# Optimization experiments

Measured on AMD Instinct MI355X. Metric: run time of the kernel, lower is better.

The kernel has to match this reference:

```python
import jax, jax.numpy as jnp
import numpy as np

DIM = 100      # number of assets in the basket
M = 50         # time steps
T = 1.0
R = 0.05
SIGMA = 0.2
S0 = 100.0
DT = T / M
H = 128        # hidden_dim of ZetaNetwork
B = 8192       # Monte-Carlo paths (batch)
EPS = 1e-5     # torch LayerNorm eps


def _layernorm(x, g, b):
    mu = jnp.mean(x, axis=-1, keepdims=True)
    var = jnp.mean((x - mu) ** 2, axis=-1, keepdims=True)
    return (x - mu) / jnp.sqrt(var + EPS) * g + b


def setup_inputs() -> dict:
    key = jax.random.key(0)
    ks = jax.random.split(key, 12)
    dw = jax.random.normal(ks[0], (B, M, DIM), dtype=jnp.float32)
    t_grid = jax.random.uniform(ks[1], (B, M), dtype=jnp.float32)
    s = 0.05
    inp = {
        "dw": dw,
        "t_grid": t_grid,
        "W1": jax.random.normal(ks[2], (DIM + 1, H), dtype=jnp.float32) * s,
        "b1": jnp.zeros((H,), jnp.float32),
        "g1": jnp.ones((H,), jnp.float32),
        "be1": jnp.zeros((H,), jnp.float32),
        "W2": jax.random.normal(ks[3], (H, H), dtype=jnp.float32) * s,
        "b2": jnp.zeros((H,), jnp.float32),
        "g2": jnp.ones((H,), jnp.float32),
        "be2": jnp.zeros((H,), jnp.float32),
        "W3": jax.random.normal(ks[4], (H, H), dtype=jnp.float32) * s,
        "b3": jnp.zeros((H,), jnp.float32),
        "g3": jnp.ones((H,), jnp.float32),
        "be3": jnp.zeros((H,), jnp.float32),
        "W4": jax.random.normal(ks[5], (H, DIM), dtype=jnp.float32) * s,
        "b4": jnp.zeros((DIM,), jnp.float32),
        "Y0": jnp.array([10.0], dtype=jnp.float32),
    }
    return inp


def reference(dw, t_grid, W1, b1, g1, be1, W2, b2, g2, be2,
              W3, b3, g3, be3, W4, b4, Y0):
    batch = dw.shape[0]

    def zeta_net(x):  # x: [B, DIM+1]
        h = jax.nn.gelu(_layernorm(x @ W1 + b1, g1, be1), approximate=False)
        h = jax.nn.gelu(_layernorm(h @ W2 + b2, g2, be2), approximate=False)
        h = jax.nn.gelu(_layernorm(h @ W3 + b3, g3, be3), approximate=False)
        return jax.nn.sigmoid(h @ W4 + b4)  # [B, DIM]

    def step(carry, xs):
        S, Y = carry
        dw_i, t_i = xs                                   # [B,DIM], [B,1]
        net_in = jnp.concatenate([S / S0, t_i], axis=1)  # [B,DIM+1]
        zeta = zeta_net(net_in)
        dS = S * (R * DT + SIGMA * dw_i)
        portfolio_gain = jnp.sum(zeta * dS, axis=1, keepdims=True)
        asset_val = jnp.sum(zeta * S, axis=1, keepdims=True)
        Y = Y + R * (Y - asset_val) * DT + portfolio_gain
        S = S + dS
        return (S, Y), None

    S_init = jnp.full((batch, DIM), S0, dtype=dw.dtype)
    Y_init = jnp.ones((batch, 1), dtype=dw.dtype) * Y0
    xs = (jnp.swapaxes(dw, 0, 1),                # [M,B,DIM]
          jnp.swapaxes(t_grid, 0, 1)[..., None])  # [M,B,1]
    (S, Y), _ = jax.lax.scan(step, (S_init, Y_init), xs)
    return (Y, S)
```

## Files before the change

### kernel.cpp

```cpp
#include <hip/hip_runtime.h>
#include <hip/hip_bf16.h>
#include <cstdint>
#include <cstddef>

typedef __attribute__((ext_vector_type(8))) short short8;
typedef __attribute__((ext_vector_type(4))) float f32x4;
typedef __attribute__((ext_vector_type(2))) float f32x2;
typedef __attribute__((ext_vector_type(4))) unsigned int u32x4;

#define NDIM 100
#define NSTEP 50
#define NPATH 8192
#define XSTR 128
#define ESTR 128

typedef const __attribute__((address_space(1))) unsigned int glb_u32;
typedef __attribute__((address_space(3))) unsigned int lds_u32;

__device__ __forceinline__ unsigned short f2b(float f){
  unsigned int u = __float_as_uint(f);
  u += 0x7fffu + ((u >> 16) & 1u);
  return (unsigned short)(u >> 16);
}
__device__ __forceinline__ float b2f(unsigned short h){
  return __uint_as_float(((unsigned int)h) << 16);
}

template<int CTRL>
__device__ __forceinline__ float dpp_add(float x){
  int t = __builtin_amdgcn_update_dpp(0, __float_as_int(x), CTRL, 0xF, 0xF, true);
  return x + __int_as_float(t);
}
__device__ __forceinline__ float rowsum16(float x){
  x = dpp_add<0x128>(x);
  x = dpp_add<0x124>(x);
  x = dpp_add<0x122>(x);
  x = dpp_add<0x121>(x);
  return x;
}

__global__ __launch_bounds__(256) void prep_weights(
    const float* __restrict__ W1, const float* __restrict__ W2,
    const float* __restrict__ W3, const float* __restrict__ W4,
    unsigned short* __restrict__ WTS)
{
  int idx = blockIdx.x * 256 + threadIdx.x;
  int j = idx & 7;
  int s = (idx >> 3) & 15;
  int n = (idx >> 7) & 127;
  int L = idx >> 14;
  int lc = s ^ (n & 15);
  int k  = j * 16 + lc;
  float v;
  if (L == 0)      v = (k <= NDIM) ? W1[k * 128 + n] : 0.f;
  else if (L == 1) v = W2[k * 128 + n];
  else if (L == 2) v = W3[k * 128 + n];
  else             v = (n < NDIM) ? W4[k * NDIM + n] : 0.f;
  WTS[idx] = f2b(v);
}

__global__ __launch_bounds__(256) void prep_params(
    const float* __restrict__ b1, const float* __restrict__ g1, const float* __restrict__ be1,
    const float* __restrict__ b2, const float* __restrict__ g2, const float* __restrict__ be2,
    const float* __restrict__ b3, const float* __restrict__ g3, const float* __restrict__ be3,
    const float* __restrict__ b4, float* __restrict__ PPAR)
{
  int idx = blockIdx.x * 256 + threadIdx.x;
  if (idx >= 1536) return;
  int ct = idx & 7;
  int c  = (idx >> 3) & 15;
  int p  = (idx >> 7) % 3;
  int L  = idx / 384;
  int col = ct * 16 + c;
  const float* v;
  if (L == 0)      v = (p == 0) ? b1 : (p == 1) ? g1 : be1;
  else if (L == 1) v = (p == 0) ? b2 : (p == 1) ? g2 : be2;
  else if (L == 2) v = (p == 0) ? b3 : (p == 1) ? g3 : be3;
  else             v = b4;
  float val;
  if (L == 3) val = (p == 0 && col < NDIM) ? b4[col] : 0.f;
  else        val = v[col];
  PPAR[idx] = val;
}

__global__ __launch_bounds__(256) void phaseA(
    const float* __restrict__ dw, const float* __restrict__ tg,
    unsigned short* __restrict__ X, unsigned short* __restrict__ E,
    float* __restrict__ Sout, int path0)
{
  const int pb = threadIdx.x >> 6;
  const int t  = threadIdx.x & 63;
  const int bl = blockIdx.x * 4 + pb;
  const int b  = path0 + bl;
  const int d0 = (t & 7) * 16 + (t >> 3);
  const int d1 = d0 + 8;
  float s0 = 100.f, s1 = 100.f;
  const float* dwb = dw + (long)b * NSTEP * NDIM;
  const float* tgb = tg + (long)b * NSTEP;
  unsigned short* Xb = X + (long)bl * NSTEP * XSTR;
  unsigned short* Eb = E + (long)bl * NSTEP * ESTR;
  for (int i = 0; i < NSTEP; ++i){
    float tv = tgb[i];
    float w0 = (d0 < NDIM) ? dwb[i * NDIM + d0] : 0.f;
    float w1 = (d1 < NDIM) ? dwb[i * NDIM + d1] : 0.f;
    unsigned short* Xr = Xb + i * XSTR;
    unsigned short* Er = Eb + i * ESTR;
    Xr[t]      = (d0 < NDIM) ? f2b(s0 * 0.01f) : ((d0 == NDIM) ? f2b(tv) : (unsigned short)0);
    Xr[t + 64] = (d1 < NDIM) ? f2b(s1 * 0.01f) : (unsigned short)0;
    Er[t]      = (d0 < NDIM) ? f2b(0.2f * s0 * w0) : (unsigned short)0;
    Er[t + 64] = (d1 < NDIM) ? f2b(0.2f * s1 * w1) : (unsigned short)0;
    s0 = fmaf(s0, 0.001f + 0.2f * w0, s0);
    s1 = fmaf(s1, 0.001f + 0.2f * w1, s1);
  }
  if (d0 < NDIM) Sout[(long)b * NDIM + d0] = s0;
  if (d1 < NDIM) Sout[(long)b * NDIM + d1] = s1;
}

__global__ __launch_bounds__(256, 3) void phaseB(
    const unsigned short* __restrict__ X,
    const unsigned short* __restrict__ E,
    const unsigned short* __restrict__ WTS,
    const float* __restrict__ PPAR,
    float* __restrict__ cbuf, long row0)
{
  __shared__ __align__(16) char lds[49152];
  char* const wbuf = lds;
  const int tid = threadIdx.x;
  const int w = tid >> 6;
  const int l = tid & 63;
  const int g = l >> 4;
  const int c = l & 15;
  char* const H = lds + 32768 + w * 4096;
  const long base = (long)blockIdx.x * 128 + w * 16;

  auto stage = [&](int Loff){
    #pragma unroll
    for (int it = 0; it < 8; ++it){
      int chunk = w * 8 + it;
      __builtin_amdgcn_global_load_lds((glb_u32*)(WTS + Loff + chunk * 512 + l * 8),
          (lds_u32*)(wbuf + chunk * 1024), 16, 0, 0);
    }
  };

  short8 af0[4], af1[4];
  {
    const unsigned short* xr0 = X + (base + c) * XSTR;
    const unsigned short* xr1 = X + (base + 64 + c) * XSTR;
    #pragma unroll
    for (int ks = 0; ks < 4; ++ks){
      af0[ks] = *(const short8*)(xr0 + 32 * ks + 8 * g);
      af1[ks] = *(const short8*)(xr1 + 32 * ks + 8 * g);
    }
  }

  auto mfma2 = [&](f32x4 (&acc0)[8], f32x4 (&acc1)[8], f32x4 blo, f32x4 bhi){
    #pragma unroll
    for (int ct = 0; ct < 8; ++ct){
      float bs = (ct < 4) ? blo[ct] : bhi[ct - 4];
      f32x4 z; z[0] = bs; z[1] = bs; z[2] = bs; z[3] = bs;
      acc0[ct] = z; acc1[ct] = z;
      const char* rowp = wbuf + ((ct * 16 + c) << 8);
      #pragma unroll
      for (int ks = 0; ks < 4; ++ks){
        short8 bf = *(const short8*)(rowp + (((4 * ks + g) ^ c) << 4));
        acc0[ct] = __builtin_amdgcn_mfma_f32_16x16x32_bf16(af0[ks], bf, acc0[ct], 0, 0, 0);
        acc1[ct] = __builtin_amdgcn_mfma_f32_16x16x32_bf16(af1[ks], bf, acc1[ct], 0, 0, 0);
      }
    }
  };

  auto gelu2 = [&](f32x2 y) -> f32x2 {
    f32x2 a = y * -2.4554673f;
    f32x2 u;
    u[0] = __builtin_amdgcn_exp2f(a[0]);
    u[1] = __builtin_amdgcn_exp2f(a[1]);
    f32x2 d = u + 1.0f;
    f32x2 r;
    r[0] = __builtin_amdgcn_rcpf(d[0]);
    r[1] = __builtin_amdgcn_rcpf(d[1]);
    return y * r;
  };

  auto postproc = [&](f32x4 (&acc)[8], short8 (&af)[4],
                      f32x4 glo, f32x4 ghi, f32x4 belo, f32x4 behi){
    f32x2 sA = {0.f, 0.f}, sB = {0.f, 0.f}, qA = {0.f, 0.f}, qB = {0.f, 0.f};
    #pragma unroll
    for (int ct = 0; ct < 8; ++ct){
      f32x2 xy = __builtin_shufflevector(acc[ct], acc[ct], 0, 1);
      f32x2 zw = __builtin_shufflevector(acc[ct], acc[ct], 2, 3);
      sA += xy; qA += xy * xy;
      sB += zw; qB += zw * zw;
    }
    sA[0] = rowsum16(sA[0]); sA[1] = rowsum16(sA[1]);
    sB[0] = rowsum16(sB[0]); sB[1] = rowsum16(sB[1]);
    qA[0] = rowsum16(qA[0]); qA[1] = rowsum16(qA[1]);
    qB[0] = rowsum16(qB[0]); qB[1] = rowsum16(qB[1]);
    f32x2 muA = sA * 0.0078125f, muB = sB * 0.0078125f;
    f32x2 vA = qA * 0.0078125f - muA * muA + 1e-5f;
    f32x2 vB = qB * 0.0078125f - muB * muB + 1e-5f;
    f32x2 rA, rB;
    rA[0] = rsqrtf(vA[0]); rA[1] = rsqrtf(vA[1]);
    rB[0] = rsqrtf(vB[0]); rB[1] = rsqrtf(vB[1]);
    u32x4 ov0, ov1, ov2, ov3;
    #pragma unroll
    for (int p = 0; p < 4; ++p){
      float ga0 = (p < 2) ? glo[2*p]     : ghi[2*p - 4];
      float ga1 = (p < 2) ? glo[2*p + 1] : ghi[2*p - 3];
      float be0 = (p < 2) ? belo[2*p]     : behi[2*p - 4];
      float be1 = (p < 2) ? belo[2*p + 1] : behi[2*p - 3];
      f32x2 xyE = __builtin_shufflevector(acc[2*p],   acc[2*p],   0, 1);
      f32x2 zwE = __builtin_shufflevector(acc[2*p],   acc[2*p],   2, 3);
      f32x2 xyO = __builtin_shufflevector(acc[2*p+1], acc[2*p+1], 0, 1);
      f32x2 zwO = __builtin_shufflevector(acc[2*p+1], acc[2*p+1], 2, 3);
      f32x2 AEA = rA * ga0, AEB = rB * ga0;
      f32x2 AOA = rA * ga1, AOB = rB * ga1;
      f32x2 hEA = gelu2(xyE * AEA + (be0 - muA * AEA));
      f32x2 hEB = gelu2(zwE * AEB + (be0 - muB * AEB));
      f32x2 hOA = gelu2(xyO * AOA + (be1 - muA * AOA));
      f32x2 hOB = gelu2(zwO * AOB + (be1 - muB * AOB));
      unsigned int k0, k1, k2, k3;
      asm("v_cvt_pk_bf16_f32 %0, %1, %2" : "=v"(k0) : "v"(hEA[0]), "v"(hOA[0]));
      asm("v_cvt_pk_bf16_f32 %0, %1, %2" : "=v"(k1) : "v"(hEA[1]), "v"(hOA[1]));
      asm("v_cvt_pk_bf16_f32 %0, %1, %2" : "=v"(k2) : "v"(hEB[0]), "v"(hOB[0]));
      asm("v_cvt_pk_bf16_f32 %0, %1, %2" : "=v"(k3) : "v"(hEB[1]), "v"(hOB[1]));
      ov0[p] = k0; ov1[p] = k1; ov2[p] = k2; ov3[p] = k3;
    }
    int r0 = 4 * g;
    *(u32x4*)(H + (r0 + 0) * 256 + ((c ^ (r0 + 0)) << 4)) = ov0;
    *(u32x4*)(H + (r0 + 1) * 256 + ((c ^ (r0 + 1)) << 4)) = ov1;
    *(u32x4*)(H + (r0 + 2) * 256 + ((c ^ (r0 + 2)) << 4)) = ov2;
    *(u32x4*)(H + (r0 + 3) * 256 + ((c ^ (r0 + 3)) << 4)) = ov3;
    #pragma unroll
    for (int ks = 0; ks < 4; ++ks)
      af[ks] = *(const short8*)(H + c * 256 + (((4 * ks + g) ^ c) << 4));
  };

  auto epilogue = [&](f32x4 (&acc)[8], short8 (&ep)[4], long rbase){
    f32x2 pgA = {0.f, 0.f}, pgB = {0.f, 0.f};
    #pragma unroll
    for (int ct = 0; ct < 8; ++ct){
      f32x2 xy = __builtin_shufflevector(acc[ct], acc[ct], 0, 1);
      f32x2 zw = __builtin_shufflevector(acc[ct], acc[ct], 2, 3);
      f32x2 aA = xy * -1.4426950f, aB = zw * -1.4426950f;
      f32x2 u, d, r;
      u[0] = __builtin_amdgcn_exp2f(aA[0]); u[1] = __builtin_amdgcn_exp2f(aA[1]);
      d = u + 1.f;
      r[0] = __builtin_amdgcn_rcpf(d[0]); r[1] = __builtin_amdgcn_rcpf(d[1]);
      f32x2 eA = { b2f((unsigned short)ep[0][ct]), b2f((unsigned short)ep[1][ct]) };
      pgA += r * eA;
      u[0] = __builtin_amdgcn_exp2f(aB[0]); u[1] = __builtin_amdgcn_exp2f(aB[1]);
      d = u + 1.f;
      r[0] = __builtin_amdgcn_rcpf(d[0]); r[1] = __builtin_amdgcn_rcpf(d[1]);
      f32x2 eB = { b2f((unsigned short)ep[2][ct]), b2f((unsigned short)ep[3][ct]) };
      pgB += r * eB;
    }
    pgA[0] = rowsum16(pgA[0]); pgA[1] = rowsum16(pgA[1]);
    pgB[0] = rowsum16(pgB[0]); pgB[1] = rowsum16(pgB[1]);
    if (c == 0){
      cbuf[row0 + rbase + 4 * g + 0] = pgA[0];
      cbuf[row0 + rbase + 4 * g + 1] = pgA[1];
      cbuf[row0 + rbase + 4 * g + 2] = pgB[0];
      cbuf[row0 + rbase + 4 * g + 3] = pgB[1];
    }
  };

  stage(0);
  __syncthreads();

  #pragma unroll
  for (int L = 0; L < 3; ++L){
    const float* pp = PPAR + L * 384 + c * 8;
    f32x4 blo  = *(const f32x4*)pp,         bhi  = *(const f32x4*)(pp + 4);
    f32x4 acc0[8], acc1[8];
    mfma2(acc0, acc1, blo, bhi);
    f32x4 glo  = *(const f32x4*)(pp + 128), ghi  = *(const f32x4*)(pp + 132);
    f32x4 belo = *(const f32x4*)(pp + 256), behi = *(const f32x4*)(pp + 260);
    __syncthreads();
    stage((L + 1) * 16384);
    postproc(acc0, af0, glo, ghi, belo, behi);
    postproc(acc1, af1, glo, ghi, belo, behi);
    __syncthreads();
  }

  {
    const float* pp = PPAR + 3 * 384 + c * 8;
    f32x4 blo = *(const f32x4*)pp, bhi = *(const f32x4*)(pp + 4);
    short8 ep0[4], ep1[4];
    #pragma unroll
    for (int j = 0; j < 4; ++j){
      ep0[j] = *(const short8*)(E + (base + 4 * g + j) * ESTR + c * 8);
      ep1[j] = *(const short8*)(E + (base + 64 + 4 * g + j) * ESTR + c * 8);
    }
    f32x4 acc0[8], acc1[8];
    mfma2(acc0, acc1, blo, bhi);
    epilogue(acc0, ep0, base);
    epilogue(acc1, ep1, base + 64);
  }
}

__global__ __launch_bounds__(256) void phaseC(const float* __restrict__ cbuf,
                                              const float* __restrict__ Y0,
                                              float* __restrict__ Yout)
{
  int b = blockIdx.x * 256 + threadIdx.x;
  if (b >= NPATH) return;
  const float kk = 1.0f + 0.05f * (1.0f / 50.0f);
  float y = Y0[0];
  const float* cb = cbuf + (long)b * NSTEP;
  #pragma unroll 10
  for (int i = 0; i < NSTEP; ++i) y = y * kk + cb[i];
  Yout[b] = y;
}

extern "C" void kernel_launch(void* const* d_in, const int* in_sizes, int n_in,
                              void* d_out, int out_size, void* d_ws, size_t ws_size,
                              hipStream_t stream)
{
  const float* dw  = (const float*)d_in[0];
  const float* tg  = (const float*)d_in[1];
  const float* W1  = (const float*)d_in[2];
  const float* b1  = (const float*)d_in[3];
  const float* g1  = (const float*)d_in[4];
  const float* be1 = (const float*)d_in[5];
  const float* W2  = (const float*)d_in[6];
  const float* b2  = (const float*)d_in[7];
  const float* g2  = (const float*)d_in[8];
  const float* be2 = (const float*)d_in[9];
  const float* W3  = (const float*)d_in[10];
  const float* b3  = (const float*)d_in[11];
  const float* g3  = (const float*)d_in[12];
  const float* be3 = (const float*)d_in[13];
  const float* W4  = (const float*)d_in[14];
  const float* b4  = (const float*)d_in[15];
  const float* Y0  = (const float*)d_in[16];
  float* out = (float*)d_out;

  char* ws = (char*)d_ws;
  unsigned short* WTS = (unsigned short*)ws;
  float* PPAR = (float*)(ws + 131072);
  float* cbuf = (float*)(ws + 137344);
  char* chunk = ws + 1775744;

  prep_weights<<<256, 256, 0, stream>>>(W1, W2, W3, W4, WTS);
  prep_params<<<6, 256, 0, stream>>>(b1, g1, be1, b2, g2, be2, b3, g3, be3, b4, PPAR);

  long avail = (long)ws_size - 1775744L;
  long pc = (avail > 0) ? (avail / 25600L) : 0;
  if (pc > 8192) pc = 8192;
  pc -= pc % 128;
  if (pc < 128) pc = 128;

  for (long p0 = 0; p0 < 8192; p0 += pc){
    long np = 8192 - p0; if (np > pc) np = pc;
    unsigned short* Xc = (unsigned short*)chunk;
    unsigned short* Ec = Xc + np * 50L * XSTR;
    phaseA<<<(int)(np / 4), 256, 0, stream>>>(dw, tg, Xc, Ec, out + 8192, (int)p0);
    long nrows = np * 50L;
    phaseB<<<(int)(nrows / 128), 256, 0, stream>>>(Xc, Ec, WTS, PPAR, cbuf, p0 * 50L);
  }
  phaseC<<<32, 256, 0, stream>>>(cbuf, Y0, out);
}
```

Baseline: 201.5 us.

## Fuse phaseA and phaseB into one software-pipelined kernel over double-buffered chunks

```diff
diff --git a/kernel.cpp b/kernel.cpp
--- a/kernel.cpp
+++ b/kernel.cpp
@@ -83,47 +83,53 @@
   PPAR[idx] = val;
 }
 
-__global__ __launch_bounds__(256) void phaseA(
+__global__ __launch_bounds__(256, 3) void fusedAB(
     const float* __restrict__ dw, const float* __restrict__ tg,
-    unsigned short* __restrict__ X, unsigned short* __restrict__ E,
-    float* __restrict__ Sout, int path0)
-{
-  const int pb = threadIdx.x >> 6;
-  const int t  = threadIdx.x & 63;
-  const int bl = blockIdx.x * 4 + pb;
-  const int b  = path0 + bl;
-  const int d0 = (t & 7) * 16 + (t >> 3);
-  const int d1 = d0 + 8;
-  float s0 = 100.f, s1 = 100.f;
-  const float* dwb = dw + (long)b * NSTEP * NDIM;
-  const float* tgb = tg + (long)b * NSTEP;
-  unsigned short* Xb = X + (long)bl * NSTEP * XSTR;
-  unsigned short* Eb = E + (long)bl * NSTEP * ESTR;
-  for (int i = 0; i < NSTEP; ++i){
-    float tv = tgb[i];
-    float w0 = (d0 < NDIM) ? dwb[i * NDIM + d0] : 0.f;
-    float w1 = (d1 < NDIM) ? dwb[i * NDIM + d1] : 0.f;
-    unsigned short* Xr = Xb + i * XSTR;
-    unsigned short* Er = Eb + i * ESTR;
-    Xr[t]      = (d0 < NDIM) ? f2b(s0 * 0.01f) : ((d0 == NDIM) ? f2b(tv) : (unsigned short)0);
-    Xr[t + 64] = (d1 < NDIM) ? f2b(s1 * 0.01f) : (unsigned short)0;
-    Er[t]      = (d0 < NDIM) ? f2b(0.2f * s0 * w0) : (unsigned short)0;
-    Er[t + 64] = (d1 < NDIM) ? f2b(0.2f * s1 * w1) : (unsigned short)0;
-    s0 = fmaf(s0, 0.001f + 0.2f * w0, s0);
-    s1 = fmaf(s1, 0.001f + 0.2f * w1, s1);
-  }
-  if (d0 < NDIM) Sout[(long)b * NDIM + d0] = s0;
-  if (d1 < NDIM) Sout[(long)b * NDIM + d1] = s1;
-}
-
-__global__ __launch_bounds__(256, 3) void phaseB(
-    const unsigned short* __restrict__ X,
-    const unsigned short* __restrict__ E,
+    unsigned short* __restrict__ XA, unsigned short* __restrict__ EA,
+    float* __restrict__ Sout, int path0A, int nA,
+    const unsigned short* __restrict__ XB,
+    const unsigned short* __restrict__ EB,
     const unsigned short* __restrict__ WTS,
     const float* __restrict__ PPAR,
-    float* __restrict__ cbuf, long row0)
+    float* __restrict__ cbuf, long row0B, int nB)
 {
   __shared__ __align__(16) char lds[49152];
+  const int s = blockIdx.x;
+  const int tot = nA + nB;
+  const int aBefore = (int)(((long)s * nA) / tot);
+  const bool isA = ((int)(((long)(s + 1) * nA) / tot)) > aBefore;
+
+  if (isA){
+    const int pb = threadIdx.x >> 6;
+    const int t  = threadIdx.x & 63;
+    const int bl = aBefore * 4 + pb;
+    const int b  = path0A + bl;
+    const int d0 = (t & 7) * 16 + (t >> 3);
+    const int d1 = d0 + 8;
+    float s0 = 100.f, s1 = 100.f;
+    const float* dwb = dw + (long)b * NSTEP * NDIM;
+    const float* tgb = tg + (long)b * NSTEP;
+    unsigned short* Xb_ = XA + (long)bl * NSTEP * XSTR;
+    unsigned short* Eb_ = EA + (long)bl * NSTEP * ESTR;
+    for (int i = 0; i < NSTEP; ++i){
+      float tv = tgb[i];
+      float w0 = (d0 < NDIM) ? dwb[i * NDIM + d0] : 0.f;
+      float w1 = (d1 < NDIM) ? dwb[i * NDIM + d1] : 0.f;
+      unsigned short* Xr = Xb_ + i * XSTR;
+      unsigned short* Er = Eb_ + i * ESTR;
+      Xr[t]      = (d0 < NDIM) ? f2b(s0 * 0.01f) : ((d0 == NDIM) ? f2b(tv) : (unsigned short)0);
+      Xr[t + 64] = (d1 < NDIM) ? f2b(s1 * 0.01f) : (unsigned short)0;
+      Er[t]      = (d0 < NDIM) ? f2b(0.2f * s0 * w0) : (unsigned short)0;
+      Er[t + 64] = (d1 < NDIM) ? f2b(0.2f * s1 * w1) : (unsigned short)0;
+      s0 = fmaf(s0, 0.001f + 0.2f * w0, s0);
+      s1 = fmaf(s1, 0.001f + 0.2f * w1, s1);
+    }
+    if (d0 < NDIM) Sout[(long)b * NDIM + d0] = s0;
+    if (d1 < NDIM) Sout[(long)b * NDIM + d1] = s1;
+    return;
+  }
+
+  const int bid = s - aBefore;
   char* const wbuf = lds;
   const int tid = threadIdx.x;
   const int w = tid >> 6;
@@ -131,7 +137,7 @@
   const int g = l >> 4;
   const int c = l & 15;
   char* const H = lds + 32768 + w * 4096;
-  const long base = (long)blockIdx.x * 128 + w * 16;
+  const long base = (long)bid * 128 + w * 16;
 
   auto stage = [&](int Loff){
     #pragma unroll
@@ -144,8 +150,8 @@
 
   short8 af0[4], af1[4];
   {
-    const unsigned short* xr0 = X + (base + c) * XSTR;
-    const unsigned short* xr1 = X + (base + 64 + c) * XSTR;
+    const unsigned short* xr0 = XB + (base + c) * XSTR;
+    const unsigned short* xr1 = XB + (base + 64 + c) * XSTR;
     #pragma unroll
     for (int ks = 0; ks < 4; ++ks){
       af0[ks] = *(const short8*)(xr0 + 32 * ks + 8 * g);
@@ -257,10 +263,10 @@
     pgA[0] = rowsum16(pgA[0]); pgA[1] = rowsum16(pgA[1]);
     pgB[0] = rowsum16(pgB[0]); pgB[1] = rowsum16(pgB[1]);
     if (c == 0){
-      cbuf[row0 + rbase + 4 * g + 0] = pgA[0];
-      cbuf[row0 + rbase + 4 * g + 1] = pgA[1];
-      cbuf[row0 + rbase + 4 * g + 2] = pgB[0];
-      cbuf[row0 + rbase + 4 * g + 3] = pgB[1];
+      cbuf[row0B + rbase + 4 * g + 0] = pgA[0];
+      cbuf[row0B + rbase + 4 * g + 1] = pgA[1];
+      cbuf[row0B + rbase + 4 * g + 2] = pgB[0];
+      cbuf[row0B + rbase + 4 * g + 3] = pgB[1];
     }
   };
 
@@ -288,8 +294,8 @@
     short8 ep0[4], ep1[4];
     #pragma unroll
     for (int j = 0; j < 4; ++j){
-      ep0[j] = *(const short8*)(E + (base + 4 * g + j) * ESTR + c * 8);
-      ep1[j] = *(const short8*)(E + (base + 64 + 4 * g + j) * ESTR + c * 8);
+      ep0[j] = *(const short8*)(EB + (base + 4 * g + j) * ESTR + c * 8);
+      ep1[j] = *(const short8*)(EB + (base + 64 + 4 * g + j) * ESTR + c * 8);
     }
     f32x4 acc0[8], acc1[8];
     mfma2(acc0, acc1, blo, bhi);
@@ -339,24 +345,32 @@
   unsigned short* WTS = (unsigned short*)ws;
   float* PPAR = (float*)(ws + 131072);
   float* cbuf = (float*)(ws + 137344);
-  char* chunk = ws + 1775744;
+  char* chunk0 = ws + 1775744;
 
   prep_weights<<<256, 256, 0, stream>>>(W1, W2, W3, W4, WTS);
   prep_params<<<6, 256, 0, stream>>>(b1, g1, be1, b2, g2, be2, b3, g3, be3, b4, PPAR);
 
   long avail = (long)ws_size - 1775744L;
-  long pc = (avail > 0) ? (avail / 25600L) : 0;
-  if (pc > 8192) pc = 8192;
+  long pc = (avail > 0) ? (avail / 51200L) : 0;
+  if (pc > 2048) pc = 2048;
   pc -= pc % 128;
   if (pc < 128) pc = 128;
 
-  for (long p0 = 0; p0 < 8192; p0 += pc){
-    long np = 8192 - p0; if (np > pc) np = pc;
-    unsigned short* Xc = (unsigned short*)chunk;
-    unsigned short* Ec = Xc + np * 50L * XSTR;
-    phaseA<<<(int)(np / 4), 256, 0, stream>>>(dw, tg, Xc, Ec, out + 8192, (int)p0);
-    long nrows = np * 50L;
-    phaseB<<<(int)(nrows / 128), 256, 0, stream>>>(Xc, Ec, WTS, PPAR, cbuf, p0 * 50L);
+  int nch = (int)((8192 + pc - 1) / pc);
+  for (int k = 0; k <= nch; ++k){
+    long p0A = (long)k * pc;
+    long npA = (k < nch) ? ((8192 - p0A) > pc ? pc : (8192 - p0A)) : 0;
+    long p0B = (long)(k - 1) * pc;
+    long npB = (k > 0) ? ((8192 - p0B) > pc ? pc : (8192 - p0B)) : 0;
+    int nA = (int)(npA / 4);
+    int nB = (int)(npB * 50L / 128L);
+    if (nA + nB == 0) continue;
+    unsigned short* Xa = (unsigned short*)(chunk0 + (long)(k & 1) * pc * 25600L);
+    unsigned short* Ea = Xa + pc * 50L * XSTR;
+    const unsigned short* Xb_ = (const unsigned short*)(chunk0 + (long)((k - 1) & 1) * pc * 25600L);
+    const unsigned short* Eb_ = Xb_ + pc * 50L * XSTR;
+    fusedAB<<<nA + nB, 256, 0, stream>>>(dw, tg, Xa, Ea, out + 8192, (int)p0A, nA,
+        Xb_, Eb_, WTS, PPAR, cbuf, p0B * 50L, nB);
   }
   phaseC<<<32, 256, 0, stream>>>(cbuf, Y0, out);
 }
```

Result: slower. 303.6 us (+50.6%).
